# Kernel tuning notes

Hardware: AMD Instinct MI355X
Metric: run time of the kernel (lower is better)

## Reference

```python
import jax, jax.numpy as jnp
import numpy as np
from jax import lax

T_STEPS = 40
BATCH = 2048
UNITS = 1024
INPUT_DIM = 1024
Q_BASIS = 8
ORDER = 4  # skfda BSpline default (cubic)


def bspline_basis(ts, q, k=ORDER):
    """Cox-de Boor B-spline basis, n_basis=q, order k, domain [0,1]. ts: (T,) -> (T,q)."""
    ts = np.asarray(ts, dtype=np.float64)
    breaks = np.linspace(0.0, 1.0, q - k + 2)
    knots = np.concatenate([np.zeros(k - 1), breaks, np.ones(k - 1)])  # len q+k
    n0 = len(knots) - 1
    N = np.zeros((len(ts), n0))
    for i in range(n0):
        N[:, i] = ((ts >= knots[i]) & (ts < knots[i + 1])).astype(np.float64)
    for d in range(1, k):
        Nn = np.zeros((len(ts), n0 - d))
        for i in range(n0 - d):
            out = np.zeros(len(ts))
            den1 = knots[i + d] - knots[i]
            if den1 > 0:
                out += (ts - knots[i]) / den1 * N[:, i]
            den2 = knots[i + d + 1] - knots[i + 1]
            if den2 > 0:
                out += (knots[i + d + 1] - ts) / den2 * N[:, i + 1]
            Nn[:, i] = out
        N = Nn
    # at right endpoint t==1 only the last basis is nonzero (value 1)
    at_end = ts >= 1.0 - 1e-12
    N[at_end] = 0.0
    N[at_end, -1] = 1.0
    return N.astype(np.float32)


def setup_inputs() -> dict:
    key = jax.random.key(0)
    k1, k2, k3 = jax.random.split(key, 3)
    D = UNITS + INPUT_DIM
    x = jax.random.normal(k1, (BATCH, T_STEPS, INPUT_DIM), dtype=jnp.float32)
    h0 = jnp.zeros((BATCH, UNITS), dtype=jnp.float32)
    Qw = jax.random.normal(k2, (D, Q_BASIS * UNITS), dtype=jnp.float32) / np.sqrt(D)
    bias = jax.random.uniform(k3, (UNITS,), dtype=jnp.float32, minval=-0.05, maxval=0.05)
    Bt_all = jnp.asarray(bspline_basis(np.linspace(0.0, 1.0, T_STEPS), Q_BASIS))
    return {"x": x, "h0": h0, "Qw": Qw, "bias": bias, "Bt_all": Bt_all}


def reference(x, h0, Qw, bias, Bt_all):
    B, T, I = x.shape
    U = h0.shape[-1]
    q = Bt_all.shape[-1]
    D = Qw.shape[0]
    # block_diag(Bt,...,Bt).T contraction == reshape Q to (D, U, q) and contract q with Bt
    Qr = Qw.reshape(D, U, q)
    W_all = jnp.einsum('duq,tq->tdu', Qr, Bt_all)  # (T, D, U) per-step weight matrices

    def step(h, xw):
        x_t, W_t = xw                       # (B,I), (D,U)
        cat = jnp.concatenate([h, x_t], axis=-1)  # (B, U+I) = (B, D); state first, as in cell
        h_new = jnp.tanh(cat @ W_t + bias)
        return h_new, h_new

    xs = jnp.swapaxes(x, 0, 1)              # (T, B, I)
    _, hs = lax.scan(step, h0, (xs, W_all))
    return jnp.swapaxes(hs, 0, 1)           # (B, T, U)
```

## Files before the change

### kernel.cpp

```cpp
#include <hip/hip_runtime.h>
#include <hip/hip_fp16.h>

#define TS 40
#define NB 2048
#define NU 1024
#define NI 1024
#define ND 2048
#define UD (1024 * 2048)

typedef _Float16 half8 __attribute__((ext_vector_type(8)));
typedef _Float16 half4v __attribute__((ext_vector_type(4)));
typedef float floatx4 __attribute__((ext_vector_type(4)));

__device__ __forceinline__ float tanh_fast(float v) {
  float e = __expf(2.0f * v);
  return 1.0f - 2.0f / (e + 1.0f);
}

__device__ __forceinline__ void gload16(const void* g, void* l) {
  __builtin_amdgcn_global_load_lds(
      (const __attribute__((address_space(1))) void*)g,
      (__attribute__((address_space(3))) void*)l, 16, 0, 0);
}

__device__ __forceinline__ int tile_off(int r, int c8) {
  return (((((r >> 4) * 2 + (c8 >> 2)) << 6) + ((c8 & 3) << 4) + (r & 15)) << 4);
}


__global__ __launch_bounds__(256) void wprep(
    const float* __restrict__ Qw, const float* __restrict__ Bt,
    _Float16* __restrict__ W)
{
  __shared__ _Float16 ldsQ[64 * 512];
  __shared__ float ldsB[TS * 8];
  const int tid = threadIdx.x;
  const int kt = blockIdx.x;
  const int ut = blockIdx.y;
  for (int i = tid; i < TS * 8; i += 256) ldsB[i] = Bt[i];
  const float* qb = Qw + (size_t)(kt * 64) * 8192 + ut * 512;
#pragma unroll
  for (int i = 0; i < 32; ++i) {
    int s = i * 256 + tid;
    int dk = s >> 7, c4 = s & 127;
    float4 v = *(const float4*)(qb + (size_t)dk * 8192 + c4 * 4);
    _Float16* d = &ldsQ[dk * 512 + c4 * 4];
    d[0] = (_Float16)v.x; d[1] = (_Float16)v.y;
    d[2] = (_Float16)v.z; d[3] = (_Float16)v.w;
  }
  __syncthreads();
  const int w = tid >> 6, lane = tid & 63;
  const int dur = lane & 7, ko = lane >> 3;
#pragma unroll 1
  for (int sp = 0; sp < 2; ++sp) {
    const int stripe = w * 2 + sp;
    const int du = stripe * 8 + dur;
    float Q[8][8];
#pragma unroll
    for (int j = 0; j < 8; ++j)
#pragma unroll
      for (int q = 0; q < 8; ++q)
        Q[j][q] = (float)ldsQ[(ko * 8 + j) * 512 + du * 8 + q];
    const int obase = tile_off(du, ko);
#pragma unroll 1
    for (int t = 0; t < TS; ++t) {
      float b[8];
#pragma unroll
      for (int q = 0; q < 8; ++q) b[q] = ldsB[t * 8 + q];
      half8 v;
#pragma unroll
      for (int j = 0; j < 8; ++j) {
        float s = 0.f;
#pragma unroll
        for (int q = 0; q < 8; ++q) s += Q[j][q] * b[q];
        v[j] = (_Float16)s;
      }
      size_t tile = ((size_t)t * 16 + ut) * 32 + kt;
      *(half8*)((char*)W + tile * 8192 + obase) = v;
    }
  }
}

__global__ __launch_bounds__(256) void hinit(const float* __restrict__ h0,
                                             _Float16* __restrict__ hb) {
  int g = blockIdx.x * 256 + threadIdx.x;
  int tile_id = g >> 9, rc = g & 511;
  int bt = tile_id >> 4, kt = tile_id & 15;
  int r = rc >> 3, c8 = rc & 7;
  const float* src = h0 + (size_t)(bt * 64 + r) * NU + kt * 64 + c8 * 8;
  float4 v0 = *(const float4*)src;
  float4 v1 = *(const float4*)(src + 4);
  half8 h;
  h[0] = (_Float16)v0.x; h[1] = (_Float16)v0.y;
  h[2] = (_Float16)v0.z; h[3] = (_Float16)v0.w;
  h[4] = (_Float16)v1.x; h[5] = (_Float16)v1.y;
  h[6] = (_Float16)v1.z; h[7] = (_Float16)v1.w;
  *(half8*)((char*)hb + (size_t)tile_id * 8192 + tile_off(r, c8)) = h;
}

__global__ __launch_bounds__(256) void xproj2(
    const float* __restrict__ x, const _Float16* __restrict__ W,
    const float* __restrict__ bias, _Float16* __restrict__ pre)
{
  __shared__ char lds[2][32768];
  const int tid = threadIdx.x;
  const int bt2 = blockIdx.x;
  const int ut2 = blockIdx.y;
  const int t   = blockIdx.z;
  const int lane = tid & 63, w = tid >> 6;
  const int wm2 = w >> 1, wn2 = w & 1;
  const int l15 = lane & 15, lk = lane >> 4;

  const float* xb = x + (size_t)(bt2 * 128) * (TS * NI) + (size_t)t * NI;
  const char* WB = (const char*)W + (((size_t)t * 16 + ut2 * 2) * 32 + 16) * 8192;

  float bv[4];
#pragma unroll
  for (int nf = 0; nf < 4; ++nf)
    bv[nf] = bias[ut2 * 128 + wn2 * 64 + nf * 16 + l15];

  float4 areg[8];

  auto loadA = [&](int p) {
#pragma unroll
    for (int i = 0; i < 8; ++i) {
      int s = i * 256 + tid;
      int r = s >> 4, c4 = s & 15;
      areg[i] = *(const float4*)(xb + (size_t)r * (TS * NI) + p * 64 + c4 * 4);
    }
  };
  auto issueB = [&](int p, int buf) {
    const char* gb = WB + (size_t)(w >> 1) * (32 * 8192) + (size_t)p * 8192 +
                     (w & 1) * 4096 + lane * 16;
    char* lb = lds[buf] + 16384 + (w >> 1) * 8192 + (w & 1) * 4096 + lane * 16;
    gload16(gb, lb);
    gload16(gb + 1024, lb + 1024);
    gload16(gb + 2048, lb + 2048);
    gload16(gb + 3072, lb + 3072);
  };
  auto writeA = [&](int buf) {
    char* pA = lds[buf];
#pragma unroll
    for (int i = 0; i < 8; ++i) {
      int s = i * 256 + tid;
      int r = s >> 4, c4 = s & 15;
      half4v h;
      h[0] = (_Float16)areg[i].x; h[1] = (_Float16)areg[i].y;
      h[2] = (_Float16)areg[i].z; h[3] = (_Float16)areg[i].w;
      *(half4v*)(pA + (r >> 6) * 8192 + tile_off(r & 63, c4 >> 1) + (c4 & 1) * 8) = h;
    }
  };

  floatx4 acc[4][4] = {};

  auto comp = [&](int buf) {
    const char* pA = lds[buf] + wm2 * 8192;
    const char* pB = lds[buf] + 16384 + wn2 * 8192;
    __builtin_amdgcn_s_setprio(1);
#pragma unroll
    for (int kk = 0; kk < 2; ++kk) {
      half8 af[4], bf[4];
#pragma unroll
      for (int mf = 0; mf < 4; ++mf)
        af[mf] = *(const half8*)(pA + (((mf * 2 + kk)) << 10) + lane * 16);
#pragma unroll
      for (int nf = 0; nf < 4; ++nf)
        bf[nf] = *(const half8*)(pB + (((nf * 2 + kk)) << 10) + lane * 16);
#pragma unroll
      for (int mf = 0; mf < 4; ++mf)
#pragma unroll
        for (int nf = 0; nf < 4; ++nf)
          acc[mf][nf] = __builtin_amdgcn_mfma_f32_16x16x32_f16(
              af[mf], bf[nf], acc[mf][nf], 0, 0, 0);
    }
    __builtin_amdgcn_s_setprio(0);
  };

  issueB(0, 0);
  loadA(0);
  writeA(0);
  __syncthreads();
#pragma unroll 1
  for (int p = 0; p < 16; ++p) {
    int cur = p & 1;
    if (p + 1 < 16) { issueB(p + 1, cur ^ 1); loadA(p + 1); }
    comp(cur);
    if (p + 1 < 16) writeA(cur ^ 1);
    __syncthreads();
  }

#pragma unroll
  for (int mf = 0; mf < 4; ++mf)
#pragma unroll
    for (int nf = 0; nf < 4; ++nf) {
      int u = ut2 * 128 + wn2 * 64 + nf * 16 + l15;
      int brow = bt2 * 128 + wm2 * 64 + mf * 16 + (lk << 2);
#pragma unroll
      for (int j = 0; j < 4; ++j)
        pre[((size_t)t * NB + brow + j) * NU + u] =
            (_Float16)(acc[mf][nf][j] + bv[nf]);
    }
}

__global__ __launch_bounds__(256) void serial2(
    const _Float16* __restrict__ Wh,
    const _Float16* __restrict__ pret,
    const _Float16* __restrict__ hprev,
    _Float16* __restrict__ hnext,
    float* __restrict__ outt)
{
  __shared__ uint4 lds4[4096];
  const int tid = threadIdx.x, bid = blockIdx.x;
  const int bt = bid & 31, ut = bid >> 5;
  const int lane = tid & 63, w = tid >> 6;
  const int wm = w >> 1, wn = w & 1;
  const int l15 = lane & 15, lk = lane >> 4;
  const int b0 = bt * 64, u0 = ut * 64;

  _Float16 pr[16];
#pragma unroll
  for (int mf = 0; mf < 2; ++mf)
#pragma unroll
    for (int nf = 0; nf < 2; ++nf)
#pragma unroll
      for (int j = 0; j < 4; ++j)
        pr[((mf * 2 + nf) << 2) + j] = pret[
            (size_t)(b0 + wm * 32 + mf * 16 + (lk << 2) + j) * NU +
            (u0 + wn * 32 + nf * 16 + l15)];

  const char* Hb = (const char*)hprev + (size_t)bt * 16 * 8192;
  const char* Wb = (const char*)Wh + (size_t)ut * 32 * 8192;

  auto issue = [&](int kt) {
    char* la = (char*)lds4 + (kt & 3) * 16384 + w * 2048;
    const char* ga = Hb + (size_t)kt * 8192 + w * 2048 + lane * 16;
    const char* gb = Wb + (size_t)kt * 8192 + w * 2048 + lane * 16;
    gload16(ga, la);
    gload16(ga + 1024, la + 1024);
    gload16(gb, la + 8192);
    gload16(gb + 1024, la + 8192 + 1024);
  };

  floatx4 acc[2][2] = {};

  issue(0);
  issue(1);
#pragma unroll 1
  for (int p = 0; p < 16; ++p) {
    if (p + 2 < 16) issue(p + 2);
    if (p < 14)       asm volatile("s_waitcnt vmcnt(8)" ::: "memory");
    else if (p == 14) asm volatile("s_waitcnt vmcnt(4)" ::: "memory");
    else              asm volatile("s_waitcnt vmcnt(0)" ::: "memory");
    __builtin_amdgcn_s_barrier();
    const char* pA = (const char*)lds4 + (p & 3) * 16384;
    const char* pB = pA + 8192;
    __builtin_amdgcn_s_setprio(1);
#pragma unroll
    for (int kk = 0; kk < 2; ++kk) {
      half8 af[2], bf[2];
#pragma unroll
      for (int mf = 0; mf < 2; ++mf)
        af[mf] = *(const half8*)(pA + ((((wm * 2 + mf) * 2 + kk) << 10) + lane * 16));
#pragma unroll
      for (int nf = 0; nf < 2; ++nf)
        bf[nf] = *(const half8*)(pB + ((((wn * 2 + nf) * 2 + kk) << 10) + lane * 16));
#pragma unroll
      for (int mf = 0; mf < 2; ++mf)
#pragma unroll
        for (int nf = 0; nf < 2; ++nf)
          acc[mf][nf] = __builtin_amdgcn_mfma_f32_16x16x32_f16(
              af[mf], bf[nf], acc[mf][nf], 0, 0, 0);
    }
    __builtin_amdgcn_s_setprio(0);
  }

#pragma unroll
  for (int mf = 0; mf < 2; ++mf)
#pragma unroll
    for (int nf = 0; nf < 2; ++nf) {
      int u = u0 + wn * 32 + nf * 16 + l15;
      int brow = b0 + wm * 32 + mf * 16 + (lk << 2);
#pragma unroll
      for (int j = 0; j < 4; ++j) {
        int b = brow + j;
        float p = (float)pr[((mf * 2 + nf) << 2) + j];
        float v = tanh_fast(acc[mf][nf][j] + p);
        outt[(size_t)b * (TS * NU) + u] = v;
        *(_Float16*)((char*)hnext + (((size_t)(bt * 16 + ut)) << 13) +
                     tile_off(b & 63, (u & 63) >> 3) + (u & 7) * 2) = (_Float16)v;
      }
    }
}

__global__ __launch_bounds__(256) void wprep_lin(
    const float* __restrict__ Qw, const float* __restrict__ Bt,
    _Float16* __restrict__ W, int t0, int nt)
{
  __shared__ float ldsQ[32 * 257];
  __shared__ float ldsB[TS * 8];
  const int tid = threadIdx.x;
  const int k0 = blockIdx.x * 32;
  const int u0 = blockIdx.y * 32;
  for (int i = tid; i < TS * 8; i += 256) ldsB[i] = Bt[i];
  const float* qbase = Qw + (size_t)k0 * 8192 + (size_t)u0 * 8;
#pragma unroll
  for (int i = 0; i < 8; ++i) {
    int s = i * 256 + tid;
    int r = s >> 6, c4 = s & 63;
    float4 v = *(const float4*)(qbase + (size_t)r * 8192 + c4 * 4);
    float* d = &ldsQ[r * 257 + c4 * 4];
    d[0] = v.x; d[1] = v.y; d[2] = v.z; d[3] = v.w;
  }
  __syncthreads();
  const int kl = tid & 31;
  const int ug = tid >> 5;
#pragma unroll
  for (int p = 0; p < 4; ++p) {
    int uu = p * 8 + ug;
    float q[8];
#pragma unroll
    for (int j = 0; j < 8; ++j) q[j] = ldsQ[kl * 257 + uu * 8 + j];
    size_t obase = (size_t)(u0 + uu) * 2048 + k0 + kl;
    for (int tt = 0; tt < nt; ++tt) {
      const float* bt = &ldsB[(t0 + tt) * 8];
      float v = 0.f;
#pragma unroll
      for (int j = 0; j < 8; ++j) v += q[j] * bt[j];
      W[(size_t)tt * UD + obase] = (_Float16)v;
    }
  }
}

__global__ __launch_bounds__(256) void step_gemm(
    const float* __restrict__ xt, const float* __restrict__ hp, long hstride,
    const _Float16* __restrict__ Wt, const float* __restrict__ bias,
    float* __restrict__ outt)
{
  __shared__ _Float16 ldsA[2][64 * 64];
  __shared__ _Float16 ldsB[2][128 * 64];
  const int tid = threadIdx.x;
  const int b0 = blockIdx.x * 64;
  const int u0 = blockIdx.y * 128;
  const int lane = tid & 63;
  const int wv = tid >> 6;
  const int wm = wv >> 1, wn = wv & 1;
  const int l15 = lane & 15, lk = lane >> 4;

  float4 areg[4];
  uint4 breg[4];

  auto stage_load = [&](int kt) {
    const int k0 = kt * 64;
    const float* src; size_t stride; int koff;
    if (k0 < NU) { src = hp; stride = (size_t)hstride; koff = k0; }
    else { src = xt; stride = (size_t)TS * NI; koff = k0 - NU; }
#pragma unroll
    for (int i = 0; i < 4; ++i) {
      int s = i * 256 + tid;
      int r = s >> 4, c4 = s & 15;
      areg[i] = *(const float4*)(src + (size_t)(b0 + r) * stride + koff + c4 * 4);
    }
    const _Float16* wsrc = Wt + (size_t)u0 * 2048 + k0;
#pragma unroll
    for (int i = 0; i < 4; ++i) {
      int s = i * 256 + tid;
      int u = s >> 3, c8 = s & 7;
      breg[i] = *(const uint4*)(wsrc + (size_t)u * 2048 + c8 * 8);
    }
  };

  auto stage_write = [&](int buf) {
    char* pA = (char*)&ldsA[buf][0];
    char* pB = (char*)&ldsB[buf][0];
#pragma unroll
    for (int i = 0; i < 4; ++i) {
      int s = i * 256 + tid;
      int r = s >> 4, c4 = s & 15;
      half4v h;
      h[0] = (_Float16)areg[i].x; h[1] = (_Float16)areg[i].y;
      h[2] = (_Float16)areg[i].z; h[3] = (_Float16)areg[i].w;
      int off = (r * 128 + c4 * 8) ^ ((r & 7) << 4);
      *(half4v*)(pA + off) = h;
    }
#pragma unroll
    for (int i = 0; i < 4; ++i) {
      int s = i * 256 + tid;
      int u = s >> 3, c8 = s & 7;
      int off = (u * 128 + c8 * 16) ^ ((u & 7) << 4);
      *(uint4*)(pB + off) = breg[i];
    }
  };

  floatx4 acc[2][4] = {};

  auto compute = [&](int buf) {
    const char* pA = (const char*)&ldsA[buf][0];
    const char* pB = (const char*)&ldsB[buf][0];
#pragma unroll
    for (int kk = 0; kk < 2; ++kk) {
      half8 af[2], bf[4];
#pragma unroll
      for (int mf = 0; mf < 2; ++mf) {
        int r = wm * 32 + mf * 16 + l15;
        int off = r * 128 + ((((kk << 2) | lk) ^ (r & 7)) << 4);
        af[mf] = *(const half8*)(pA + off);
      }
#pragma unroll
      for (int nf = 0; nf < 4; ++nf) {
        int u = wn * 64 + nf * 16 + l15;
        int off = u * 128 + ((((kk << 2) | lk) ^ (u & 7)) << 4);
        bf[nf] = *(const half8*)(pB + off);
      }
#pragma unroll
      for (int mf = 0; mf < 2; ++mf)
#pragma unroll
        for (int nf = 0; nf < 4; ++nf)
          acc[mf][nf] =
              __builtin_amdgcn_mfma_f32_16x16x32_f16(af[mf], bf[nf], acc[mf][nf], 0, 0, 0);
    }
  };

  stage_load(0);
  stage_write(0);
  __syncthreads();
#pragma unroll 1
  for (int kt = 0; kt < 32; ++kt) {
    int cur = kt & 1;
    if (kt + 1 < 32) stage_load(kt + 1);
    compute(cur);
    if (kt + 1 < 32) stage_write(cur ^ 1);
    __syncthreads();
  }

#pragma unroll
  for (int mf = 0; mf < 2; ++mf)
#pragma unroll
    for (int nf = 0; nf < 4; ++nf) {
      int u = u0 + wn * 64 + nf * 16 + l15;
      float bv = bias[u];
      int brow = b0 + wm * 32 + mf * 16 + (lk << 2);
#pragma unroll
      for (int j = 0; j < 4; ++j) {
        float prev = acc[mf][nf][j] + bv;
        outt[(size_t)(brow + j) * (TS * NU) + u] = tanh_fast(prev);
      }
    }
}

extern "C" void kernel_launch(void* const* d_in, const int* in_sizes, int n_in,
                              void* d_out, int out_size, void* d_ws, size_t ws_size,
                              hipStream_t stream) {
  const float* x    = (const float*)d_in[0];
  const float* h0   = (const float*)d_in[1];
  const float* Qw   = (const float*)d_in[2];
  const float* bias = (const float*)d_in[3];
  const float* Bt   = (const float*)d_in[4];
  float* out = (float*)d_out;

  char* ws = (char*)d_ws;
  const size_t w_bytes    = (size_t)UD * TS * sizeof(_Float16);
  const size_t pre_bytes  = (size_t)TS * NB * NU * sizeof(_Float16);
  const size_t slot_bytes = (size_t)NB * NU * sizeof(_Float16);
  const size_t need = w_bytes + pre_bytes + 2 * slot_bytes;

  if (ws_size >= need) {
    _Float16* W   = (_Float16*)ws;
    _Float16* pre = (_Float16*)(ws + w_bytes);
    _Float16* hb  = (_Float16*)(ws + w_bytes + pre_bytes);
    const size_t SLOT = (size_t)NB * NU;

    wprep<<<dim3(32, 16), 256, 0, stream>>>(Qw, Bt, W);
    hinit<<<dim3(1024), 256, 0, stream>>>(h0, hb);
    xproj2<<<dim3(16, 8, TS), 256, 0, stream>>>(x, W, bias, pre);

    for (int t = 0; t < TS; ++t) {
      const _Float16* hprev = hb + (size_t)(t & 1) * SLOT;
      _Float16* hnext = hb + (size_t)((t + 1) & 1) * SLOT;
      serial2<<<dim3(512), 256, 0, stream>>>(
          W + (size_t)t * UD, pre + (size_t)t * NB * NU, hprev, hnext,
          out + (size_t)t * NU);
    }
  } else {
    _Float16* W = (_Float16*)ws;
    const bool big = ws_size >= w_bytes;
    if (big) wprep_lin<<<dim3(64, 32), 256, 0, stream>>>(Qw, Bt, W, 0, TS);
    for (int t = 0; t < TS; ++t) {
      const _Float16* Wtp;
      if (big) {
        Wtp = W + (size_t)t * UD;
      } else {
        wprep_lin<<<dim3(64, 32), 256, 0, stream>>>(Qw, Bt, W, t, 1);
        Wtp = W;
      }
      const float* hp = (t == 0) ? h0 : out + (size_t)(t - 1) * NU;
      long hstride = (t == 0) ? NU : (long)TS * NU;
      step_gemm<<<dim3(32, 8), 256, 0, stream>>>(
          x + (size_t)t * NI, hp, hstride, Wtp, bias, out + (size_t)t * NU);
    }
  }
}
```

Measured before the change: 949.6 us.

## Pre-tile x to fp16, use direct-to-LDS loads, tile pre and coalesce h writes

Adds an xprep kernel that converts x to fp16 in the tiled MFMA layout, so the input projection can stream both operands with global_load_lds instead of doing per-thread fp32 loads and conversions. The projection output and the recurrent state are staged through LDS and written as contiguous 16-byte tiles instead of scattered 2-byte stores. serial3 loads its pre-activation tile through LDS and deepens prefetching to three stages. The cost is an extra pass over x and more workspace.

```diff
diff --git a/kernel.cpp b/kernel.cpp
--- a/kernel.cpp
+++ b/kernel.cpp
@@ -78,6 +78,42 @@
       size_t tile = ((size_t)t * 16 + ut) * 32 + kt;
       *(half8*)((char*)W + tile * 8192 + obase) = v;
     }
+  }
+}
+
+__global__ __launch_bounds__(256) void xprep(
+    const float* __restrict__ x, _Float16* __restrict__ X)
+{
+  __shared__ char stage[8192];
+  const int tid = threadIdx.x;
+  const int bt = blockIdx.x, t = blockIdx.y;
+  char* outb = (char*)X + ((size_t)(t * 32 + bt) * 16) * 8192;
+  const int r = tid >> 2, cq = tid & 3;
+#pragma unroll 1
+  for (int kt = 0; kt < 16; ++kt) {
+    const float* src =
+        x + (size_t)(bt * 64 + r) * (TS * NI) + (size_t)t * NI + kt * 64 + cq * 16;
+    float4 a0 = *(const float4*)(src);
+    float4 a1 = *(const float4*)(src + 4);
+    float4 a2 = *(const float4*)(src + 8);
+    float4 a3 = *(const float4*)(src + 12);
+    half8 h0, h1;
+    h0[0] = (_Float16)a0.x; h0[1] = (_Float16)a0.y;
+    h0[2] = (_Float16)a0.z; h0[3] = (_Float16)a0.w;
+    h0[4] = (_Float16)a1.x; h0[5] = (_Float16)a1.y;
+    h0[6] = (_Float16)a1.z; h0[7] = (_Float16)a1.w;
+    h1[0] = (_Float16)a2.x; h1[1] = (_Float16)a2.y;
+    h1[2] = (_Float16)a2.z; h1[3] = (_Float16)a2.w;
+    h1[4] = (_Float16)a3.x; h1[5] = (_Float16)a3.y;
+    h1[6] = (_Float16)a3.z; h1[7] = (_Float16)a3.w;
+    *(half8*)(stage + tile_off(r, cq * 2)) = h0;
+    *(half8*)(stage + tile_off(r, cq * 2 + 1)) = h1;
+    __syncthreads();
+    uint4 v0 = *(const uint4*)(stage + tid * 32);
+    uint4 v1 = *(const uint4*)(stage + tid * 32 + 16);
+    *(uint4*)(outb + (size_t)kt * 8192 + tid * 32) = v0;
+    *(uint4*)(outb + (size_t)kt * 8192 + tid * 32 + 16) = v1;
+    __syncthreads();
   }
 }
 
@@ -98,11 +134,11 @@
   *(half8*)((char*)hb + (size_t)tile_id * 8192 + tile_off(r, c8)) = h;
 }
 
-__global__ __launch_bounds__(256) void xproj2(
-    const float* __restrict__ x, const _Float16* __restrict__ W,
+__global__ __launch_bounds__(256) void xproj3(
+    const _Float16* __restrict__ X, const _Float16* __restrict__ W,
     const float* __restrict__ bias, _Float16* __restrict__ pre)
 {
-  __shared__ char lds[2][32768];
+  __shared__ char lds[65536];
   const int tid = threadIdx.x;
   const int bt2 = blockIdx.x;
   const int ut2 = blockIdx.y;
@@ -111,61 +147,39 @@
   const int wm2 = w >> 1, wn2 = w & 1;
   const int l15 = lane & 15, lk = lane >> 4;
 
-  const float* xb = x + (size_t)(bt2 * 128) * (TS * NI) + (size_t)t * NI;
-  const char* WB = (const char*)W + (((size_t)t * 16 + ut2 * 2) * 32 + 16) * 8192;
+  const char* Xb = (const char*)X + (((size_t)t * 32 + bt2 * 2) * 16) * 8192;
+  const char* Wb = (const char*)W + (((size_t)t * 16 + ut2 * 2) * 32 + 16) * 8192;
 
   float bv[4];
 #pragma unroll
   for (int nf = 0; nf < 4; ++nf)
     bv[nf] = bias[ut2 * 128 + wn2 * 64 + nf * 16 + l15];
 
-  float4 areg[8];
-
-  auto loadA = [&](int p) {
-#pragma unroll
-    for (int i = 0; i < 8; ++i) {
-      int s = i * 256 + tid;
-      int r = s >> 4, c4 = s & 15;
-      areg[i] = *(const float4*)(xb + (size_t)r * (TS * NI) + p * 64 + c4 * 4);
-    }
+  auto issue = [&](int p) {
+    const char* src = (w < 2)
+        ? Xb + (size_t)w * (16 * 8192) + (size_t)p * 8192
+        : Wb + (size_t)(w - 2) * (32 * 8192) + (size_t)p * 8192;
+    src += lane * 16;
+    char* dst = lds + (p & 1) * 32768 + w * 8192;
+#pragma unroll
+    for (int i = 0; i < 8; ++i) gload16(src + i * 1024, dst + i * 1024);
   };
-  auto issueB = [&](int p, int buf) {
-    const char* gb = WB + (size_t)(w >> 1) * (32 * 8192) + (size_t)p * 8192 +
-                     (w & 1) * 4096 + lane * 16;
-    char* lb = lds[buf] + 16384 + (w >> 1) * 8192 + (w & 1) * 4096 + lane * 16;
-    gload16(gb, lb);
-    gload16(gb + 1024, lb + 1024);
-    gload16(gb + 2048, lb + 2048);
-    gload16(gb + 3072, lb + 3072);
-  };
-  auto writeA = [&](int buf) {
-    char* pA = lds[buf];
-#pragma unroll
-    for (int i = 0; i < 8; ++i) {
-      int s = i * 256 + tid;
-      int r = s >> 4, c4 = s & 15;
-      half4v h;
-      h[0] = (_Float16)areg[i].x; h[1] = (_Float16)areg[i].y;
-      h[2] = (_Float16)areg[i].z; h[3] = (_Float16)areg[i].w;
-      *(half4v*)(pA + (r >> 6) * 8192 + tile_off(r & 63, c4 >> 1) + (c4 & 1) * 8) = h;
-    }
-  };
 
   floatx4 acc[4][4] = {};
 
-  auto comp = [&](int buf) {
-    const char* pA = lds[buf] + wm2 * 8192;
-    const char* pB = lds[buf] + 16384 + wn2 * 8192;
+  auto comp = [&](int p) {
+    const char* pA = lds + (p & 1) * 32768 + wm2 * 8192;
+    const char* pB = lds + (p & 1) * 32768 + 16384 + wn2 * 8192;
     __builtin_amdgcn_s_setprio(1);
 #pragma unroll
     for (int kk = 0; kk < 2; ++kk) {
       half8 af[4], bf[4];
 #pragma unroll
       for (int mf = 0; mf < 4; ++mf)
-        af[mf] = *(const half8*)(pA + (((mf * 2 + kk)) << 10) + lane * 16);
+        af[mf] = *(const half8*)(pA + ((mf * 2 + kk) << 10) + lane * 16);
 #pragma unroll
       for (int nf = 0; nf < 4; ++nf)
-        bf[nf] = *(const half8*)(pB + (((nf * 2 + kk)) << 10) + lane * 16);
+        bf[nf] = *(const half8*)(pB + ((nf * 2 + kk) << 10) + lane * 16);
 #pragma unroll
       for (int mf = 0; mf < 4; ++mf)
 #pragma unroll
@@ -176,40 +190,55 @@
     __builtin_amdgcn_s_setprio(0);
   };
 
-  issueB(0, 0);
-  loadA(0);
-  writeA(0);
-  __syncthreads();
+  issue(0);
 #pragma unroll 1
   for (int p = 0; p < 16; ++p) {
-    int cur = p & 1;
-    if (p + 1 < 16) { issueB(p + 1, cur ^ 1); loadA(p + 1); }
-    comp(cur);
-    if (p + 1 < 16) writeA(cur ^ 1);
-    __syncthreads();
-  }
-
+    if (p + 1 < 16) {
+      issue(p + 1);
+      asm volatile("s_waitcnt vmcnt(8)" ::: "memory");
+    } else {
+      asm volatile("s_waitcnt vmcnt(0)" ::: "memory");
+    }
+    __builtin_amdgcn_s_barrier();
+    comp(p);
+    __builtin_amdgcn_s_barrier();
+  }
+
+  __syncthreads();
 #pragma unroll
   for (int mf = 0; mf < 4; ++mf)
 #pragma unroll
-    for (int nf = 0; nf < 4; ++nf) {
-      int u = ut2 * 128 + wn2 * 64 + nf * 16 + l15;
-      int brow = bt2 * 128 + wm2 * 64 + mf * 16 + (lk << 2);
-#pragma unroll
-      for (int j = 0; j < 4; ++j)
-        pre[((size_t)t * NB + brow + j) * NU + u] =
-            (_Float16)(acc[mf][nf][j] + bv[nf]);
-    }
-}
-
-__global__ __launch_bounds__(256) void serial2(
+    for (int nf = 0; nf < 4; ++nf)
+#pragma unroll
+      for (int j = 0; j < 4; ++j) {
+        int bl = mf * 16 + (lk << 2) + j;
+        int ul = nf * 16 + l15;
+        int c8 = ul >> 3;
+        int off = (wm2 * 2 + wn2) * 8192 + tile_off(bl, c8) + (ul & 7) * 2;
+        *(_Float16*)(lds + off) = (_Float16)(acc[mf][nf][j] + bv[nf]);
+      }
+  __syncthreads();
+#pragma unroll
+  for (int q4 = 0; q4 < 4; ++q4) {
+    int tb = q4 >> 1, tu = q4 & 1;
+    char* gdst = (char*)pre +
+        (((size_t)t * 32 + bt2 * 2 + tb) * 16 + ut2 * 2 + tu) * 8192;
+#pragma unroll
+    for (int i = 0; i < 2; ++i) {
+      uint4 v = *(const uint4*)(lds + q4 * 8192 + i * 4096 + tid * 16);
+      *(uint4*)(gdst + (size_t)i * 4096 + tid * 16) = v;
+    }
+  }
+}
+
+__global__ __launch_bounds__(256) void serial3(
     const _Float16* __restrict__ Wh,
     const _Float16* __restrict__ pret,
     const _Float16* __restrict__ hprev,
     _Float16* __restrict__ hnext,
     float* __restrict__ outt)
 {
-  __shared__ uint4 lds4[4096];
+  __shared__ uint4 lds4[4608];
   const int tid = threadIdx.x, bid = blockIdx.x;
   const int bt = bid & 31, ut = bid >> 5;
   const int lane = tid & 63, w = tid >> 6;
@@ -217,16 +246,13 @@
   const int l15 = lane & 15, lk = lane >> 4;
   const int b0 = bt * 64, u0 = ut * 64;
 
-  _Float16 pr[16];
-#pragma unroll
-  for (int mf = 0; mf < 2; ++mf)
-#pragma unroll
-    for (int nf = 0; nf < 2; ++nf)
-#pragma unroll
-      for (int j = 0; j < 4; ++j)
-        pr[((mf * 2 + nf) << 2) + j] = pret[
-            (size_t)(b0 + wm * 32 + mf * 16 + (lk << 2) + j) * NU +
-            (u0 + wn * 32 + nf * 16 + l15)];
+  {
+    const char* src = (const char*)pret + ((size_t)(bt * 16 + ut)) * 8192 +
+                      w * 2048 + lane * 16;
+    char* dst = (char*)(lds4 + 4096) + w * 2048;
+    gload16(src, dst);
+    gload16(src + 1024, dst + 1024);
+  }
 
   const char* Hb = (const char*)hprev + (size_t)bt * 16 * 8192;
   const char* Wb = (const char*)Wh + (size_t)ut * 32 * 8192;
@@ -245,13 +271,14 @@
 
   issue(0);
   issue(1);
+  issue(2);
 #pragma unroll 1
   for (int p = 0; p < 16; ++p) {
-    if (p + 2 < 16) issue(p + 2);
     if (p < 14)       asm volatile("s_waitcnt vmcnt(8)" ::: "memory");
     else if (p == 14) asm volatile("s_waitcnt vmcnt(4)" ::: "memory");
     else              asm volatile("s_waitcnt vmcnt(0)" ::: "memory");
     __builtin_amdgcn_s_barrier();
+    if (p + 3 < 16) issue(p + 3);
     const char* pA = (const char*)lds4 + (p & 3) * 16384;
     const char* pB = pA + 8192;
     __builtin_amdgcn_s_setprio(1);
@@ -274,22 +301,31 @@
     __builtin_amdgcn_s_setprio(0);
   }
 
+  __syncthreads();
+  const char* pl = (const char*)(lds4 + 4096);
 #pragma unroll
   for (int mf = 0; mf < 2; ++mf)
 #pragma unroll
-    for (int nf = 0; nf < 2; ++nf) {
-      int u = u0 + wn * 32 + nf * 16 + l15;
-      int brow = b0 + wm * 32 + mf * 16 + (lk << 2);
+    for (int nf = 0; nf < 2; ++nf)
 #pragma unroll
       for (int j = 0; j < 4; ++j) {
-        int b = brow + j;
-        float p = (float)pr[((mf * 2 + nf) << 2) + j];
-        float v = tanh_fast(acc[mf][nf][j] + p);
-        outt[(size_t)b * (TS * NU) + u] = v;
-        *(_Float16*)((char*)hnext + (((size_t)(bt * 16 + ut)) << 13) +
-                     tile_off(b & 63, (u & 63) >> 3) + (u & 7) * 2) = (_Float16)v;
-      }
-    }
+        int bl = wm * 32 + mf * 16 + (lk << 2) + j;
+        int ul = wn * 32 + nf * 16 + l15;
+        int c8 = ul >> 3;
+        int off = tile_off(bl, c8) + (ul & 7) * 2;
+        float pv = (float)*(const _Float16*)(pl + off);
+        float v = tanh_fast(acc[mf][nf][j] + pv);
+        outt[(size_t)(b0 + bl) * (TS * NU) + u0 + ul] = v;
+        *(_Float16*)((char*)lds4 + off) = (_Float16)v;
+      }
+  __syncthreads();
+  {
+    char* gdst = (char*)hnext + ((size_t)(bt * 16 + ut)) * 8192;
+    uint4 v0 = *((const uint4*)lds4 + tid * 2);
+    uint4 v1 = *((const uint4*)lds4 + tid * 2 + 1);
+    *(uint4*)(gdst + (size_t)tid * 32) = v0;
+    *(uint4*)(gdst + (size_t)tid * 32 + 16) = v1;
+  }
 }
 
 __global__ __launch_bounds__(256) void wprep_lin(
@@ -459,25 +495,28 @@
 
   char* ws = (char*)d_ws;
   const size_t w_bytes    = (size_t)UD * TS * sizeof(_Float16);
-  const size_t pre_bytes  = (size_t)TS * NB * NU * sizeof(_Float16);
+  const size_t x_bytes    = w_bytes;
+  const size_t pre_bytes  = w_bytes;
   const size_t slot_bytes = (size_t)NB * NU * sizeof(_Float16);
-  const size_t need = w_bytes + pre_bytes + 2 * slot_bytes;
+  const size_t need = w_bytes + x_bytes + pre_bytes + 2 * slot_bytes;
 
   if (ws_size >= need) {
     _Float16* W   = (_Float16*)ws;
-    _Float16* pre = (_Float16*)(ws + w_bytes);
-    _Float16* hb  = (_Float16*)(ws + w_bytes + pre_bytes);
+    _Float16* X   = (_Float16*)(ws + w_bytes);
+    _Float16* pre = (_Float16*)(ws + w_bytes + x_bytes);
+    _Float16* hb  = (_Float16*)(ws + w_bytes + x_bytes + pre_bytes);
     const size_t SLOT = (size_t)NB * NU;
 
     wprep<<<dim3(32, 16), 256, 0, stream>>>(Qw, Bt, W);
+    xprep<<<dim3(32, 40), 256, 0, stream>>>(x, X);
     hinit<<<dim3(1024), 256, 0, stream>>>(h0, hb);
-    xproj2<<<dim3(16, 8, TS), 256, 0, stream>>>(x, W, bias, pre);
+    xproj3<<<dim3(16, 8, TS), 256, 0, stream>>>(X, W, bias, pre);
 
     for (int t = 0; t < TS; ++t) {
       const _Float16* hprev = hb + (size_t)(t & 1) * SLOT;
       _Float16* hnext = hb + (size_t)((t + 1) & 1) * SLOT;
-      serial2<<<dim3(512), 256, 0, stream>>>(
-          W + (size_t)t * UD, pre + (size_t)t * NB * NU, hprev, hnext,
+      serial3<<<dim3(512), 256, 0, stream>>>(
+          W + (size_t)t * UD, pre + (size_t)t * SLOT, hprev, hnext,
           out + (size_t)t * NU);
     }
   } else {
```

After: 1.002 ms. 1.05x slower.
